# Kernel tuning notes

Hardware: AMD Instinct MI355X
Metric: run time of the kernel (lower is better)

## Reference

```python
import jax, jax.numpy as jnp
import numpy as np

KNN = 16
EPS = 1e-5

def _bn(x, g, b):
    # BatchNorm2d over channel-last axis, training-mode batch stats (axes B,N,K)
    m = jnp.mean(x, axis=(0, 1, 2), keepdims=True)
    v = jnp.var(x, axis=(0, 1, 2), keepdims=True)
    return (x - m) * jax.lax.rsqrt(v + EPS) * g + b

def _gather(x, idx):
    # x [B,N,C], idx [B,...] -> [B,...,C]
    return jax.vmap(lambda xi, ii: xi[ii])(x, idx)

def _fps(pc, m):
    # deterministic farthest point sampling starting at index 0 -> [B,m] int32
    B, N, _ = pc.shape
    first = jnp.zeros((B,), jnp.int32)
    def body(carry, _):
        mind, last = carry
        lp = jnp.take_along_axis(pc, last[:, None, None], axis=1)  # [B,1,3]
        mind = jnp.minimum(mind, jnp.sum((pc - lp) ** 2, axis=-1))  # [B,N]
        nxt = jnp.argmax(mind, axis=-1).astype(jnp.int32)
        return (mind, nxt), nxt
    _, rest = jax.lax.scan(body, (jnp.full((B, N), 1e10, pc.dtype), first), None, length=m - 1)
    return jnp.concatenate([first[None], rest], axis=0).T  # [B,m]

def _knn(pc1, pc2, k):
    # squared-distance matrix + k smallest (sorted ascending) -> indices [B,N1,k]
    d = (jnp.sum(pc1 ** 2, -1)[:, :, None] + jnp.sum(pc2 ** 2, -1)[:, None, :]
         - 2.0 * jnp.einsum('bnc,bmc->bnm', pc1, pc2))
    return jax.lax.top_k(-d, k)[1]

def reference(dec_x, dec_pc, enc_x, enc_pc,
              W_pre1, b_pre1, W_pre2, b_pre2,
              Wq, bq, Wk, bk, Wv, bv,
              Wp1, bp1, gp, betap, Wp2, bp2,
              Wa1, ba1, ga, betaa, Wa2, ba2,
              W_post1, b_post1, W_post2, b_post2):
    residue = dec_x
    dx = dec_x @ W_pre1 + b_pre1
    ex = enc_x @ W_pre2 + b_pre2
    pc = jnp.concatenate([dec_pc, enc_pc], axis=1)
    xx = jnp.concatenate([dx, ex], axis=1)
    fidx = _fps(pc, dec_pc.shape[1])
    pc = _gather(pc, fidx)
    xx = _gather(xx, fidx)
    q = dx @ Wq + bq
    k = xx @ Wk + bk
    v = xx @ Wv + bv
    nidx = _knn(dec_pc, pc, KNN)                          # [B,N1,K]
    pos_in = _gather(pc, nidx) - dec_pc[:, :, None, :]    # [B,N1,K,3] relative pos
    k = _gather(k, nidx)                                  # [B,N1,K,D]
    v = _gather(v, nidx)
    pos = jax.nn.relu(_bn(pos_in @ Wp1 + bp1, gp, betap)) @ Wp2 + bp2
    attn = k - q[:, :, None, :] + pos
    attn = jax.nn.relu(_bn(attn @ Wa1 + ba1, ga, betaa)) @ Wa2 + ba2
    attn = jax.nn.softmax(attn, axis=-2)                  # softmax over K neighbors
    x = jnp.sum((v + pos) * attn, axis=2)                 # [B,N1,D]
    return (x @ W_post1 + b_post1 + residue, dec_pc, x @ W_post2 + b_post2, enc_pc)

def setup_inputs():
    B, N1, N2 = 4, 2048, 2048
    D, I1, I2, HP, HA = 256, 256, 256, 64, 64
    ks = jax.random.split(jax.random.key(0), 24)
    rn = lambda i, shp, s: jax.random.normal(ks[i], shp, jnp.float32) * s
    z = lambda n: jnp.zeros((n,), jnp.float32)
    o = lambda n: jnp.ones((n,), jnp.float32)
    return {
        'dec_x': rn(0, (B, N1, I1), 1.0),
        'dec_pc': jax.random.uniform(ks[1], (B, N1, 3), jnp.float32),
        'enc_x': rn(2, (B, N2, I2), 1.0),
        'enc_pc': jax.random.uniform(ks[3], (B, N2, 3), jnp.float32),
        'W_pre1': rn(4, (I1, D), 0.02), 'b_pre1': z(D),
        'W_pre2': rn(5, (I2, D), 0.02), 'b_pre2': z(D),
        'Wq': rn(6, (D, D), 0.02), 'bq': z(D),
        'Wk': rn(7, (D, D), 0.02), 'bk': z(D),
        'Wv': rn(8, (D, D), 0.02), 'bv': z(D),
        'Wp1': rn(9, (3, HP), 0.1), 'bp1': z(HP), 'gp': o(HP), 'betap': z(HP),
        'Wp2': rn(10, (HP, D), 0.02), 'bp2': z(D),
        'Wa1': rn(11, (D, HA), 0.02), 'ba1': z(HA), 'ga': o(HA), 'betaa': z(HA),
        'Wa2': rn(12, (HA, D), 0.02), 'ba2': z(D),
        'W_post1': rn(13, (D, I1), 0.02), 'b_post1': z(I1),
        'W_post2': rn(14, (D, I2), 0.02), 'b_post2': z(I2),
    }
```

## Files before the change

### kernel.cpp

```cpp
#include <hip/hip_runtime.h>
#include <hip/hip_bf16.h>


typedef __hip_bfloat16 bf16;

__device__ __forceinline__ float b2f(bf16 x){ return __bfloat162float(x); }
__device__ __forceinline__ bf16  f2b(float x){ return __float2bfloat16(x); }

#define NQ    8192
#define NSAMP 131072

__global__ void detect_dtype(const unsigned int* __restrict__ words,
                             int* __restrict__ flag)
{
  int i = blockIdx.x*256 + threadIdx.x;
  unsigned int w = words[i];
  float v = __uint_as_float((w & 0xffffu) << 16);
  if (!(fabsf(v) <= 1e3f)) atomicOr(flag, 1);
}

struct ConvArgs {
  const void* src[30];
  float*      dst[30];
  int         n[30];
};
__global__ void convert_inputs(ConvArgs a, const int* __restrict__ flag)
{
  int t = blockIdx.y;
  int n = a.n[t];
  int isf32 = *flag;
  const void* s = a.src[t];
  float* d = a.dst[t];
  for (int i = blockIdx.x*256 + threadIdx.x; i < n; i += gridDim.x*256) {
    d[i] = isf32 ? ((const float*)s)[i] : b2f(((const bf16*)s)[i]);
  }
}

struct SGemm { float As[16][68]; float Bs[16][68]; };
struct SFps  { float sx[4096]; float sy[4096]; float sz[4096]; float2 slot[2][4]; };
union  SMega { SGemm g; SFps f; };

__device__ __forceinline__ void gemm_body(
    SGemm& sm, const float* __restrict__ A, const float* __restrict__ W,
    const float* __restrict__ bias, const float* __restrict__ resid,
    float* __restrict__ C, int N, int bm, int bn)
{
  int tid = threadIdx.x;
  int tr = tid >> 4, tc = tid & 15;
  float acc[4][4] = {};
  for (int k0 = 0; k0 < 256; k0 += 16) {
#pragma unroll
    for (int i = 0; i < 4; ++i) {
      int idx = tid + i*256;
      int m = idx >> 4, k = idx & 15;
      sm.As[k][m] = A[(size_t)(bm+m)*256 + k0 + k];
    }
#pragma unroll
    for (int i = 0; i < 4; ++i) {
      int idx = tid + i*256;
      int k = idx >> 6, n = idx & 63;
      sm.Bs[k][n] = W[(size_t)(k0+k)*N + bn + n];
    }
    __syncthreads();
#pragma unroll
    for (int k = 0; k < 16; ++k) {
      float4 a4 = *(const float4*)&sm.As[k][tr*4];
      float4 b4 = *(const float4*)&sm.Bs[k][tc*4];
      float a[4] = {a4.x, a4.y, a4.z, a4.w};
      float b[4] = {b4.x, b4.y, b4.z, b4.w};
#pragma unroll
      for (int i = 0; i < 4; ++i)
#pragma unroll
        for (int j = 0; j < 4; ++j) acc[i][j] += a[i]*b[j];
    }
    __syncthreads();
  }
#pragma unroll
  for (int i = 0; i < 4; ++i) {
    int m = bm + tr*4 + i;
#pragma unroll
    for (int j = 0; j < 4; ++j) {
      int n = bn + tc*4 + j;
      float v = acc[i][j];
      if (bias)  v += bias[n];
      if (resid) v += resid[(size_t)m*N + n];
      C[(size_t)m*N + n] = v;
    }
  }
}

template<int CTRL>
__device__ __forceinline__ void dpp_step(float& d, int& i) {
  int sd = __builtin_amdgcn_update_dpp(__float_as_int(d), __float_as_int(d),
                                       CTRL, 0xf, 0xf, false);
  int si = __builtin_amdgcn_update_dpp(i, i, CTRL, 0xf, 0xf, false);
  float fd = __int_as_float(sd);
  bool take = (fd > d) || (fd == d && si < i);
  d = take ? fd : d;
  i = take ? si : i;
}

__device__ void fps_body(SFps& sm, int b,
                         const float* __restrict__ dec_pc,
                         const float* __restrict__ enc_pc,
                         int* __restrict__ fidx)
{
  int tid = threadIdx.x;
  float px[16], py[16], pz[16], mind[16];
#pragma unroll
  for (int i = 0; i < 16; ++i) {
    int p = tid*16 + i;
    const float* s = (p < 2048) ? dec_pc + ((size_t)b*2048 + p)*3
                                : enc_pc + ((size_t)b*2048 + (p-2048))*3;
    px[i] = s[0]; py[i] = s[1]; pz[i] = s[2];
    sm.sx[p] = px[i]; sm.sy[p] = py[i]; sm.sz[p] = pz[i];
    mind[i] = 1e10f;
  }
  if (tid == 0) fidx[(size_t)b*2048] = 0;
  __syncthreads();

  int last = 0;
  int wv = tid >> 6;
  for (int t = 1; t < 2048; ++t) {
    float lx = sm.sx[last], ly = sm.sy[last], lz = sm.sz[last];
#pragma unroll
    for (int i = 0; i < 16; ++i) {
      float ddx = px[i]-lx, ddy = py[i]-ly, ddz = pz[i]-lz;
      float d = __fadd_rn(__fadd_rn(__fmul_rn(ddx,ddx), __fmul_rn(ddy,ddy)),
                          __fmul_rn(ddz,ddz));
      mind[i] = fminf(mind[i], d);
    }
    float vd[8]; int vi[8];
#pragma unroll
    for (int j = 0; j < 8; ++j) {
      bool tk = mind[j+8] > mind[j];
      vd[j] = tk ? mind[j+8] : mind[j];
      vi[j] = tk ? (j+8) : j;
    }
#pragma unroll
    for (int j = 0; j < 4; ++j) {
      bool tk = vd[j+4] > vd[j];
      vd[j] = tk ? vd[j+4] : vd[j];
      vi[j] = tk ? vi[j+4] : vi[j];
    }
#pragma unroll
    for (int j = 0; j < 2; ++j) {
      bool tk = vd[j+2] > vd[j];
      vd[j] = tk ? vd[j+2] : vd[j];
      vi[j] = tk ? vi[j+2] : vi[j];
    }
    bool tk0 = vd[1] > vd[0];
    float bv = tk0 ? vd[1] : vd[0];
    int   bi = tid*16 + (tk0 ? vi[1] : vi[0]);
    dpp_step<0x111>(bv, bi);
    dpp_step<0x112>(bv, bi);
    dpp_step<0x114>(bv, bi);
    dpp_step<0x118>(bv, bi);
    dpp_step<0x142>(bv, bi);
    dpp_step<0x143>(bv, bi);
    int par = t & 1;
    if ((tid & 63) == 63) sm.slot[par][wv] = make_float2(bv, __int_as_float(bi));
    __syncthreads();
    float4 s01 = *(const float4*)&sm.slot[par][0];
    float4 s23 = *(const float4*)&sm.slot[par][2];
    float d0 = s01.x; int i0 = __float_as_int(s01.y);
    float d1 = s01.z; int i1 = __float_as_int(s01.w);
    float d2 = s23.x; int i2 = __float_as_int(s23.y);
    float d3 = s23.z; int i3 = __float_as_int(s23.w);
    if (d1 > d0) { d0 = d1; i0 = i1; }
    if (d3 > d2) { d2 = d3; i2 = i3; }
    if (d2 > d0) { d0 = d2; i0 = i2; }
    last = i0;
    if (tid == 0) fidx[(size_t)b*2048 + t] = i0;
  }
}

struct Mega1Args {
  const float *dec_pc, *enc_pc, *dec_x, *enc_x;
  const float *WfV1, *WfV2, *WfQ, *WfK1, *WfK2;
  const float *bfV1, *bfV2, *bfQ, *bfK1, *bfK2;
  float *vdec, *venc, *qab, *kdec, *kenc;
  float *out1, *out3;
  int *fidx;
};
__global__ __launch_bounds__(256) void mega1(Mega1Args a)
{
  __shared__ SMega sm;
  int id = blockIdx.x;
  if (id < 4) {
    fps_body(sm.f, id, a.dec_pc, a.enc_pc, a.fidx);
  } else if (id < 516) {
    int l = id - 4;
    gemm_body(sm.g, a.dec_x, a.WfV1, a.bfV1, nullptr, a.vdec, 256,
              (l & 127) << 6, (l >> 7) << 6);
  } else if (id < 1028) {
    int l = id - 516;
    gemm_body(sm.g, a.enc_x, a.WfV2, a.bfV2, nullptr, a.venc, 256,
              (l & 127) << 6, (l >> 7) << 6);
  } else if (id < 1156) {
    int l = id - 1028;
    gemm_body(sm.g, a.dec_x, a.WfQ, a.bfQ, nullptr, a.qab, 64, l << 6, 0);
  } else if (id < 1284) {
    int l = id - 1156;
    gemm_body(sm.g, a.dec_x, a.WfK1, a.bfK1, nullptr, a.kdec, 64, l << 6, 0);
  } else if (id < 1412) {
    int l = id - 1284;
    gemm_body(sm.g, a.enc_x, a.WfK2, a.bfK2, nullptr, a.kenc, 64, l << 6, 0);
  } else if (id < 1508) {
    int i = (id - 1412)*256 + threadIdx.x;
    a.out1[i] = a.dec_pc[i];
  } else {
    int i = (id - 1508)*256 + threadIdx.x;
    a.out3[i] = a.enc_pc[i];
  }
}

__global__ __launch_bounds__(64) void foldA(
    const float* __restrict__ Wq, const float* __restrict__ bq,
    const float* __restrict__ Wk, const float* __restrict__ bk,
    const float* __restrict__ Wa1,
    const float* __restrict__ Wp2, const float* __restrict__ bp2,
    const float* __restrict__ ba1,
    float* __restrict__ Wqa, float* __restrict__ Wka,
    float* __restrict__ bqa, float* __restrict__ bka,
    float* __restrict__ Wpr, float* __restrict__ c1)
{
  int c = threadIdx.x;
  int r = blockIdx.x;
  if (r < 257) {
    float aq = 0.f, ak = 0.f;
    if (r < 256) {
      for (int j = 0; j < 256; ++j) {
        float w = Wa1[j*64+c];
        aq += Wq[r*256+j]*w; ak += Wk[r*256+j]*w;
      }
      Wqa[r*64+c] = aq; Wka[r*64+c] = ak;
    } else {
      for (int j = 0; j < 256; ++j) {
        float w = Wa1[j*64+c];
        aq += bq[j]*w; ak += bk[j]*w;
      }
      bqa[c] = aq; bka[c] = ak;
    }
  } else {
    int rr = r - 257;
    if (rr < 64) {
      float acc = 0.f;
      for (int e = 0; e < 256; ++e) acc += Wp2[rr*256+e] * Wa1[e*64+c];
      Wpr[rr*64+c] = acc;
    } else {
      float acc = ba1[c];
      for (int e = 0; e < 256; ++e) acc += bp2[e] * Wa1[e*64+c];
      c1[c] = acc;
    }
  }
}

struct FoldBArgs {
  const float *W_pre1, *W_pre2, *Wv, *Wqa, *Wka;
  const float *b_pre1, *b_pre2, *bv, *bqa, *bka;
  float *WfV1, *WfV2, *WfQ, *WfK1, *WfK2;
  float *bfV1, *bfV2, *bfQ, *bfK1, *bfK2;
};
__global__ __launch_bounds__(256) void foldB(FoldBArgs a)
{
  __shared__ SGemm sm;
  int id = blockIdx.x;
  if (id < 16) {
    gemm_body(sm, a.W_pre1, a.Wv, nullptr, nullptr, a.WfV1, 256,
              (id & 3) << 6, (id >> 2) << 6);
  } else if (id < 32) {
    int l = id - 16;
    gemm_body(sm, a.W_pre2, a.Wv, nullptr, nullptr, a.WfV2, 256,
              (l & 3) << 6, (l >> 2) << 6);
  } else if (id < 36) {
    gemm_body(sm, a.W_pre1, a.Wqa, nullptr, nullptr, a.WfQ, 64, (id-32) << 6, 0);
  } else if (id < 40) {
    gemm_body(sm, a.W_pre1, a.Wka, nullptr, nullptr, a.WfK1, 64, (id-36) << 6, 0);
  } else if (id < 44) {
    gemm_body(sm, a.W_pre2, a.Wka, nullptr, nullptr, a.WfK2, 64, (id-40) << 6, 0);
  } else {
    int t = threadIdx.x;
    float s1 = 0.f, s2 = 0.f;
    for (int k = 0; k < 256; ++k) {
      float w = a.Wv[k*256+t];
      s1 += a.b_pre1[k]*w; s2 += a.b_pre2[k]*w;
    }
    a.bfV1[t] = s1 + a.bv[t];
    a.bfV2[t] = s2 + a.bv[t];
    if (t < 64) {
      float q = 0.f, k1 = 0.f, k2 = 0.f;
      for (int k = 0; k < 256; ++k) {
        float wq = a.Wqa[k*64+t], wk = a.Wka[k*64+t];
        q  += a.b_pre1[k]*wq;
        k1 += a.b_pre1[k]*wk;
        k2 += a.b_pre2[k]*wk;
      }
      a.bfQ[t]  = q  + a.bqa[t];
      a.bfK1[t] = k1 + a.bka[t];
      a.bfK2[t] = k2 + a.bka[t];
    }
  }
}

__global__ __launch_bounds__(64) void gfetch(
    const float* __restrict__ vdec, const float* __restrict__ venc,
    const float* __restrict__ kdec, const float* __restrict__ kenc,
    const float* __restrict__ dec_pc, const float* __restrict__ enc_pc,
    const int* __restrict__ fidx,
    float* __restrict__ vsb, float* __restrict__ kab, float* __restrict__ pcs)
{
  int id = blockIdx.x;
  if (id < 8192) {
    int r = id;
    int b = r >> 11;
    int g = fidx[r];
    const float* vsrc = (g < 2048) ? vdec + ((size_t)(b*2048 + g))*256
                                   : venc + ((size_t)(b*2048 + g - 2048))*256;
    ((float4*)(vsb + (size_t)r*256))[threadIdx.x] = ((const float4*)vsrc)[threadIdx.x];
    const float* ksrc = (g < 2048) ? kdec + (size_t)(b*2048 + g)*64
                                   : kenc + (size_t)(b*2048 + g - 2048)*64;
    kab[(size_t)r*64 + threadIdx.x] = ksrc[threadIdx.x];
  } else {
    int i = (id - 8192)*64 + threadIdx.x;
    int b = i >> 11;
    int g = fidx[i];
    const float* s = (g < 2048) ? dec_pc + ((size_t)b*2048 + g)*3
                                : enc_pc + ((size_t)b*2048 + (g-2048))*3;
    float X = s[0], Y = s[1], Z = s[2];
    float s2 = __fadd_rn(__fadd_rn(__fmul_rn(X,X), __fmul_rn(Y,Y)), __fmul_rn(Z,Z));
    ((float4*)pcs)[i] = make_float4(X, Y, Z, s2);
  }
}

__global__ __launch_bounds__(64) void knn_kernel(
    const float* __restrict__ dec_pc, const float* __restrict__ pcs,
    int* __restrict__ nidx)
{
  int gq = blockIdx.x*64 + threadIdx.x;
  if (gq >= NQ) return;
  int b = gq >> 11;
  float qx = dec_pc[(size_t)gq*3+0];
  float qy = dec_pc[(size_t)gq*3+1];
  float qz = dec_pc[(size_t)gq*3+2];
  float s1 = __fadd_rn(__fadd_rn(__fmul_rn(qx,qx), __fmul_rn(qy,qy)), __fmul_rn(qz,qz));
  float bd[16]; int bi[16];
#pragma unroll
  for (int i = 0; i < 16; ++i) { bd[i] = 3.4e38f; bi[i] = 0; }
  const float4* P = (const float4*)(pcs) + (size_t)b*2048;
  for (int j = 0; j < 2048; ++j) {
    float4 p = P[j];
    float inner = __fadd_rn(__fadd_rn(__fmul_rn(qx,p.x), __fmul_rn(qy,p.y)),
                            __fmul_rn(qz,p.z));
    float d = __fsub_rn(__fadd_rn(s1, p.w), __fmul_rn(2.f, inner));
    if (d < bd[15]) {
      bd[15] = d; bi[15] = j;
#pragma unroll
      for (int k = 15; k >= 1; --k) {
        if (bd[k] < bd[k-1]) {
          float td = bd[k]; bd[k] = bd[k-1]; bd[k-1] = td;
          int   ti = bi[k]; bi[k] = bi[k-1]; bi[k-1] = ti;
        }
      }
    }
  }
  int* o = nidx + (size_t)gq*16;
#pragma unroll
  for (int i = 0; i < 16; ++i) o[i] = bi[i];
}

__global__ __launch_bounds__(256) void bn1_stats(
    const float* __restrict__ dec_pc, const float* __restrict__ pcs,
    const int* __restrict__ nidx, const float* __restrict__ Wp1,
    const float* __restrict__ bp1, double* __restrict__ sums)
{
  __shared__ float pin[256][3];
  __shared__ float red[8][64];
  int tid = threadIdx.x;
  int s0 = blockIdx.x * 256;
  {
    int s = s0 + tid;
    int qrow = s >> 4;
    int b = s >> 15;
    int g = nidx[s];
    float4 p = ((const float4*)pcs)[(size_t)b*2048 + g];
    pin[tid][0] = p.x - dec_pc[(size_t)qrow*3+0];
    pin[tid][1] = p.y - dec_pc[(size_t)qrow*3+1];
    pin[tid][2] = p.z - dec_pc[(size_t)qrow*3+2];
  }
  __syncthreads();
  int c = tid & 63, grp = tid >> 6;
  float w0 = Wp1[c], w1 = Wp1[64+c], w2 = Wp1[128+c], bb = bp1[c];
  float sm = 0.f, sq = 0.f;
  for (int i = 0; i < 64; ++i) {
    int r = grp*64 + i;
    float h = pin[r][0]*w0 + pin[r][1]*w1 + pin[r][2]*w2 + bb;
    sm += h; sq += h*h;
  }
  red[grp][c] = sm; red[4+grp][c] = sq;
  __syncthreads();
  if (tid < 64) {
    atomicAdd(&sums[tid], (double)(red[0][tid]+red[1][tid]+red[2][tid]+red[3][tid]));
  } else if (tid < 128) {
    int c2 = tid - 64;
    atomicAdd(&sums[64+c2], (double)(red[4][c2]+red[5][c2]+red[6][c2]+red[7][c2]));
  }
}

__global__ void bn_fin(const double* __restrict__ sums,
                       const float* __restrict__ gamma, const float* __restrict__ beta,
                       float* __restrict__ ab)
{
  int c = threadIdx.x;
  double mean = sums[c]    * (1.0/131072.0);
  double var  = sums[64+c] * (1.0/131072.0) - mean*mean;
  double inv  = 1.0 / sqrt(var + 1e-5);
  float a  = (float)(gamma[c] * inv);
  float bb = (float)(beta[c] - mean * (double)a);
  ab[c] = a; ab[64+c] = bb;
}

__global__ __launch_bounds__(256) void ph_kernel(
    const float* __restrict__ dec_pc, const float* __restrict__ pcs,
    const int* __restrict__ nidx, const float* __restrict__ Wp1,
    const float* __restrict__ bp1, const float* __restrict__ ab,
    bf16* __restrict__ PH)
{
  __shared__ float pin[256][3];
  int tid = threadIdx.x;
  int s0 = blockIdx.x * 256;
  {
    int s = s0 + tid;
    int qrow = s >> 4;
    int b = s >> 15;
    int g = nidx[s];
    float4 p = ((const float4*)pcs)[(size_t)b*2048 + g];
    pin[tid][0] = p.x - dec_pc[(size_t)qrow*3+0];
    pin[tid][1] = p.y - dec_pc[(size_t)qrow*3+1];
    pin[tid][2] = p.z - dec_pc[(size_t)qrow*3+2];
  }
  __syncthreads();
  int c = tid & 63, grp = tid >> 6;
  float w0 = Wp1[c], w1 = Wp1[64+c], w2 = Wp1[128+c], bb = bp1[c];
  float a = ab[c], sh = ab[64+c];
  for (int i = 0; i < 64; ++i) {
    int r = grp*64 + i;
    int s = s0 + r;
    float h = pin[r][0]*w0 + pin[r][1]*w1 + pin[r][2]*w2 + bb;
    PH[(size_t)s*64 + c] = f2b(fmaxf(h*a + sh, 0.f));
  }
}

__global__ __launch_bounds__(256) void bn2_stats(
    const bf16* __restrict__ PH, const float* __restrict__ Wpr,
    const float* __restrict__ ka, const float* __restrict__ qa,
    const float* __restrict__ c1v, const int* __restrict__ nidx,
    bf16* __restrict__ attnpre, double* __restrict__ sums)
{
  __shared__ float phT[64][68];
  __shared__ float wp[64][68];
  __shared__ float red[16][64];
  __shared__ float red2[16][64];
  int tid = threadIdx.x;
  int s0 = blockIdx.x * 64;
#pragma unroll
  for (int i = 0; i < 16; ++i) {
    int idx = tid + i*256;
    wp[idx>>6][idx&63] = Wpr[idx];
    int r = idx >> 6, d = idx & 63;
    phT[d][r] = b2f(PH[(size_t)(s0+r)*64 + d]);
  }
  __syncthreads();
  int tr = tid >> 4, tc = tid & 15;
  float acc[4][4] = {};
#pragma unroll 8
  for (int d = 0; d < 64; ++d) {
    float4 a4 = *(const float4*)&phT[d][tr*4];
    float4 b4 = *(const float4*)&wp[d][tc*4];
    float a[4] = {a4.x, a4.y, a4.z, a4.w};
    float b[4] = {b4.x, b4.y, b4.z, b4.w};
#pragma unroll
    for (int i = 0; i < 4; ++i)
#pragma unroll
      for (int j = 0; j < 4; ++j) acc[i][j] += a[i]*b[j];
  }
  float psum[4] = {0,0,0,0}, psq[4] = {0,0,0,0};
#pragma unroll
  for (int i = 0; i < 4; ++i) {
    int r = tr*4 + i;
    int s = s0 + r;
    int qrow = s >> 4;
    const float* karow = ka + (size_t)s*64;
    const float* qarow = qa + (size_t)qrow*64;
    (void)karow;
#pragma unroll
    for (int j = 0; j < 4; ++j) {
      int c = tc*4 + j;
      int b = s >> 15;
      int g = nidx[s];
      float v = acc[i][j] + ka[((size_t)(b*2048 + g))*64 + c] - qarow[c] + c1v[c];
      attnpre[(size_t)s*64 + c] = f2b(v);
      psum[j] += v; psq[j] += v*v;
    }
  }
#pragma unroll
  for (int j = 0; j < 4; ++j) { red[tr][tc*4+j] = psum[j]; red2[tr][tc*4+j] = psq[j]; }
  __syncthreads();
  if (tid < 64) {
    float t = 0.f, t2 = 0.f;
#pragma unroll
    for (int i = 0; i < 16; ++i) { t += red[i][tid]; t2 += red2[i][tid]; }
    atomicAdd(&sums[tid], (double)t);
    atomicAdd(&sums[64+tid], (double)t2);
  }
}

__global__ __launch_bounds__(256) void final_attn(
    const bf16* __restrict__ attnpre, const bf16* __restrict__ PH,
    const float* __restrict__ ab2,
    const float* __restrict__ Wa2, const float* __restrict__ ba2,
    const float* __restrict__ Wp2, const float* __restrict__ bp2,
    const float* __restrict__ vsb, const int* __restrict__ nidx,
    float* __restrict__ xout)
{
  int tid = threadIdx.x;
  float wa[64], wpc[64];
#pragma unroll
  for (int d = 0; d < 64; ++d) {
    wa[d]  = Wa2[d*256 + tid];
    wpc[d] = Wp2[d*256 + tid];
  }
  float cba2 = ba2[tid];
  float cbp2 = bp2[tid];
  __shared__ float th[16][64];
  __shared__ float ph[16][64];
  __shared__ int   sn[16];
  for (int qi = 0; qi < 16; ++qi) {
    int q = blockIdx.x*16 + qi;
#pragma unroll
    for (int i = 0; i < 4; ++i) {
      int idx = tid + i*256;
      int k = idx >> 6, d = idx & 63;
      size_t gi = (size_t)q*1024 + idx;
      th[k][d] = fmaxf(b2f(attnpre[gi])*ab2[d] + ab2[64+d], 0.f);
      ph[k][d] = b2f(PH[gi]);
    }
    if (tid < 16) sn[tid] = nidx[(size_t)q*16 + tid];
    __syncthreads();
    float av[16], pv[16];
#pragma unroll
    for (int k = 0; k < 16; ++k) {
      float sa = cba2, sp = cbp2;
#pragma unroll
      for (int d = 0; d < 64; d += 4) {
        float4 t4 = *(const float4*)&th[k][d];
        float4 p4 = *(const float4*)&ph[k][d];
        sa += t4.x*wa[d] + t4.y*wa[d+1] + t4.z*wa[d+2] + t4.w*wa[d+3];
        sp += p4.x*wpc[d] + p4.y*wpc[d+1] + p4.z*wpc[d+2] + p4.w*wpc[d+3];
      }
      av[k] = sa; pv[k] = sp;
    }
    float m = av[0];
#pragma unroll
    for (int k = 1; k < 16; ++k) m = fmaxf(m, av[k]);
    float den = 0.f, num = 0.f;
    int b = q >> 11;
#pragma unroll
    for (int k = 0; k < 16; ++k) {
      float e = __expf(av[k] - m);
      den += e;
      float vk = vsb[((size_t)(b*2048 + sn[k]))*256 + tid];
      num += (vk + pv[k]) * e;
    }
    xout[(size_t)q*256 + tid] = num / den;
    __syncthreads();
  }
}

struct PostArgs {
  const float *xb, *Wp1_, *bp1_, *Wp2_, *bp2_, *resid;
  float *o1, *o2;
};
__global__ __launch_bounds__(256) void mega_post(PostArgs a)
{
  __shared__ SGemm sm;
  int id = blockIdx.x;
  if (id < 512) {
    gemm_body(sm, a.xb, a.Wp1_, a.bp1_, a.resid, a.o1, 256,
              (id & 127) << 6, (id >> 7) << 6);
  } else {
    int l = id - 512;
    gemm_body(sm, a.xb, a.Wp2_, a.bp2_, nullptr, a.o2, 256,
              (l & 127) << 6, (l >> 7) << 6);
  }
}

extern "C" void kernel_launch(void* const* d_in, const int* in_sizes, int n_in,
                              void* d_out, int out_size, void* d_ws, size_t ws_size,
                              hipStream_t stream) {
  (void)in_sizes; (void)n_in; (void)out_size; (void)ws_size;
  char* ws = (char*)d_ws;

  float* vdec    = (float*)(ws + 0);
  float* venc    = (float*)(ws + 8388608);
  float* vsb     = (float*)(ws + 16777216);
  float* xb      = (float*)(ws + 25165824);
  float* dec_xF  = (float*)(ws + 33554432);
  float* enc_xF  = (float*)(ws + 41943040);
  bf16*  PHb     = (bf16*)(ws + 50331648);
  bf16*  apre    = (bf16*)(ws + 67108864);
  float* qab     = (float*)(ws + 83886080);
  float* kab     = (float*)(ws + 85983232);
  float* kdec    = (float*)(ws + 88080384);
  float* kenc    = (float*)(ws + 90177536);
  float* dec_pcF = (float*)(ws + 92274688);
  float* enc_pcF = (float*)(ws + 92372992);
  float* W_pre1F = (float*)(ws + 92471296);
  float* W_pre2F = (float*)(ws + 92733440);
  float* WqF     = (float*)(ws + 92995584);
  float* WkF     = (float*)(ws + 93257728);
  float* WvF     = (float*)(ws + 93519872);
  float* W_post1F= (float*)(ws + 93782016);
  float* W_post2F= (float*)(ws + 94044160);
  float* Wp2F    = (float*)(ws + 94306304);
  float* Wa1F    = (float*)(ws + 94371840);
  float* Wa2F    = (float*)(ws + 94437376);
  float* Wp1F    = (float*)(ws + 94502912);
  float* vecs    = (float*)(ws + 94503680);
  float* b_pre1F = vecs + 0*256;
  float* b_pre2F = vecs + 1*256;
  float* bqF     = vecs + 2*256;
  float* bkF     = vecs + 3*256;
  float* bvF     = vecs + 4*256;
  float* bp1F    = vecs + 5*256;
  float* gpF     = vecs + 6*256;
  float* betapF  = vecs + 7*256;
  float* bp2F    = vecs + 8*256;
  float* ba1F    = vecs + 9*256;
  float* gaF     = vecs + 10*256;
  float* betaaF  = vecs + 11*256;
  float* ba2F    = vecs + 12*256;
  float* b_post1F= vecs + 13*256;
  float* b_post2F= vecs + 14*256;
  float* WfV1    = (float*)(ws + 94519040);
  float* WfV2    = (float*)(ws + 94781184);
  float* WfQ     = (float*)(ws + 95043328);
  float* WfK1    = (float*)(ws + 95108864);
  float* WfK2    = (float*)(ws + 95174400);
  float* Wqa     = (float*)(ws + 95239936);
  float* Wka     = (float*)(ws + 95305472);
  float* bfV1    = (float*)(ws + 95371008);
  float* bfV2    = (float*)(ws + 95372032);
  float* bfQ     = (float*)(ws + 95373056);
  float* bfK1    = (float*)(ws + 95373312);
  float* bfK2    = (float*)(ws + 95373568);
  float* bqa     = (float*)(ws + 95373824);
  float* bka     = (float*)(ws + 95374080);
  float* pcs     = (float*)(ws + 95374336);
  int*   fidx    = (int*)(ws + 95505408);
  int*   nidx    = (int*)(ws + 95538176);
  double* sums   = (double*)(ws + 96062464);
  float* Wpr     = (float*)(ws + 96064512);
  float* c1v     = (float*)(ws + 96080896);
  float* a1b1    = (float*)(ws + 96081152);
  float* a2b2    = (float*)(ws + 96081664);
  int*   flag    = (int*)(ws + 96082176);

  float* out  = (float*)d_out;
  float* out1 = out + 2097152;
  float* out2 = out + 2121728;
  float* out3 = out + 4218880;

  hipMemsetAsync(sums, 0, 256*sizeof(double), stream);
  hipMemsetAsync(flag, 0, sizeof(int), stream);

  detect_dtype<<<64, 256, 0, stream>>>((const unsigned int*)d_in[2], flag);

  ConvArgs ca;
  const int ns[30] = {2097152,24576,2097152,24576, 65536,256,65536,256,
                      65536,256,65536,256,65536,256, 192,64,64,64,
                      16384,256,16384,64,64,64,16384,256,
                      65536,256,65536,256};
  float* dsts[30] = {dec_xF,dec_pcF,enc_xF,enc_pcF, W_pre1F,b_pre1F,W_pre2F,b_pre2F,
                     WqF,bqF,WkF,bkF,WvF,bvF, Wp1F,bp1F,gpF,betapF,
                     Wp2F,bp2F,Wa1F,ba1F,gaF,betaaF,Wa2F,ba2F,
                     W_post1F,b_post1F,W_post2F,b_post2F};
  for (int i = 0; i < 30; ++i) { ca.src[i] = d_in[i]; ca.dst[i] = dsts[i]; ca.n[i] = ns[i]; }
  convert_inputs<<<dim3(512, 30), 256, 0, stream>>>(ca, flag);

  foldA<<<322, 64, 0, stream>>>(WqF, bqF, WkF, bkF, Wa1F, Wp2F, bp2F, ba1F,
                                Wqa, Wka, bqa, bka, Wpr, c1v);

  FoldBArgs fb;
  fb.W_pre1 = W_pre1F; fb.W_pre2 = W_pre2F; fb.Wv = WvF; fb.Wqa = Wqa; fb.Wka = Wka;
  fb.b_pre1 = b_pre1F; fb.b_pre2 = b_pre2F; fb.bv = bvF; fb.bqa = bqa; fb.bka = bka;
  fb.WfV1 = WfV1; fb.WfV2 = WfV2; fb.WfQ = WfQ; fb.WfK1 = WfK1; fb.WfK2 = WfK2;
  fb.bfV1 = bfV1; fb.bfV2 = bfV2; fb.bfQ = bfQ; fb.bfK1 = bfK1; fb.bfK2 = bfK2;
  foldB<<<45, 256, 0, stream>>>(fb);

  Mega1Args m1;
  m1.dec_pc = dec_pcF; m1.enc_pc = enc_pcF; m1.dec_x = dec_xF; m1.enc_x = enc_xF;
  m1.WfV1 = WfV1; m1.WfV2 = WfV2; m1.WfQ = WfQ; m1.WfK1 = WfK1; m1.WfK2 = WfK2;
  m1.bfV1 = bfV1; m1.bfV2 = bfV2; m1.bfQ = bfQ; m1.bfK1 = bfK1; m1.bfK2 = bfK2;
  m1.vdec = vdec; m1.venc = venc; m1.qab = qab; m1.kdec = kdec; m1.kenc = kenc;
  m1.out1 = out1; m1.out3 = out3; m1.fidx = fidx;
  mega1<<<1604, 256, 0, stream>>>(m1);

  gfetch<<<8320, 64, 0, stream>>>(vdec, venc, kdec, kenc, dec_pcF, enc_pcF,
                                  fidx, vsb, kab, pcs);
  knn_kernel<<<128, 64, 0, stream>>>(dec_pcF, pcs, nidx);

  bn1_stats<<<512, 256, 0, stream>>>(dec_pcF, pcs, nidx, Wp1F, bp1F, sums);
  bn_fin<<<1, 64, 0, stream>>>(sums, gpF, betapF, a1b1);
  ph_kernel<<<512, 256, 0, stream>>>(dec_pcF, pcs, nidx, Wp1F, bp1F, a1b1, PHb);

  bn2_stats<<<2048, 256, 0, stream>>>(PHb, Wpr, kab, qab, c1v, nidx, apre, sums + 128);
  bn_fin<<<1, 64, 0, stream>>>(sums + 128, gaF, betaaF, a2b2);

  final_attn<<<512, 256, 0, stream>>>(apre, PHb, a2b2, Wa2F, ba2F, Wp2F, bp2F,
                                      vsb, nidx, xb);

  PostArgs pa;
  pa.xb = xb; pa.Wp1_ = W_post1F; pa.bp1_ = b_post1F;
  pa.Wp2_ = W_post2F; pa.bp2_ = b_post2F; pa.resid = dec_xF;
  pa.o1 = out; pa.o2 = out2;
  mega_post<<<1024, 256, 0, stream>>>(pa);
}
```

Baseline: 2.765 ms.

## Use 512-thread blocks for FPS and GEMMs and fold BN finalization into consumers

Farthest point sampling now runs with 512 threads, each owning 8 points instead of 16, so each serial iteration has shorter per-thread min and argmax chains. Point coordinates are packed as float4 in shared memory and the next point is fetched right after the cross-wave reduction. FPS also raises its wave priority with s_setprio. The shared GEMM body is remapped to 512 threads computing 2x4 outputs each, so the mega1, foldB and mega_post launches change to 512 threads. The two tiny bn_fin kernels are removed and their mean/variance finalization is recomputed inside ph_kernel and final_attn, saving two launches. The cost is a wider block barrier across 8 waves per FPS step and duplicated per-thread double-precision finalization.

```diff
diff --git a/kernel.cpp b/kernel.cpp
--- a/kernel.cpp
+++ b/kernel.cpp
@@ -37,7 +37,10 @@
 }
 
 struct SGemm { float As[16][68]; float Bs[16][68]; };
-struct SFps  { float sx[4096]; float sy[4096]; float sz[4096]; float2 slot[2][4]; };
+struct SFps  {
+  float4 spc[4096];
+  __align__(16) float2 slot[2][8];
+};
 union  SMega { SGemm g; SFps f; };
 
 __device__ __forceinline__ void gemm_body(
@@ -47,37 +50,33 @@
 {
   int tid = threadIdx.x;
   int tr = tid >> 4, tc = tid & 15;
-  float acc[4][4] = {};
+  float acc[2][4] = {};
   for (int k0 = 0; k0 < 256; k0 += 16) {
 #pragma unroll
-    for (int i = 0; i < 4; ++i) {
-      int idx = tid + i*256;
+    for (int i = 0; i < 2; ++i) {
+      int idx = tid + i*512;
       int m = idx >> 4, k = idx & 15;
       sm.As[k][m] = A[(size_t)(bm+m)*256 + k0 + k];
-    }
-#pragma unroll
-    for (int i = 0; i < 4; ++i) {
-      int idx = tid + i*256;
-      int k = idx >> 6, n = idx & 63;
-      sm.Bs[k][n] = W[(size_t)(k0+k)*N + bn + n];
+      int kb = idx >> 6, n = idx & 63;
+      sm.Bs[kb][n] = W[(size_t)(k0+kb)*N + bn + n];
     }
     __syncthreads();
 #pragma unroll
     for (int k = 0; k < 16; ++k) {
-      float4 a4 = *(const float4*)&sm.As[k][tr*4];
+      float2 a2 = *(const float2*)&sm.As[k][tr*2];
       float4 b4 = *(const float4*)&sm.Bs[k][tc*4];
-      float a[4] = {a4.x, a4.y, a4.z, a4.w};
+      float a[2] = {a2.x, a2.y};
       float b[4] = {b4.x, b4.y, b4.z, b4.w};
 #pragma unroll
-      for (int i = 0; i < 4; ++i)
+      for (int i = 0; i < 2; ++i)
 #pragma unroll
         for (int j = 0; j < 4; ++j) acc[i][j] += a[i]*b[j];
     }
     __syncthreads();
   }
 #pragma unroll
-  for (int i = 0; i < 4; ++i) {
-    int m = bm + tr*4 + i;
+  for (int i = 0; i < 2; ++i) {
+    int m = bm + tr*2 + i;
 #pragma unroll
     for (int j = 0; j < 4; ++j) {
       int n = bn + tc*4 + j;
@@ -105,53 +104,51 @@
                          const float* __restrict__ enc_pc,
                          int* __restrict__ fidx)
 {
+#if defined(__has_builtin)
+#if __has_builtin(__builtin_amdgcn_s_setprio)
+  __builtin_amdgcn_s_setprio(3);
+#endif
+#endif
   int tid = threadIdx.x;
-  float px[16], py[16], pz[16], mind[16];
-#pragma unroll
-  for (int i = 0; i < 16; ++i) {
-    int p = tid*16 + i;
+  float px[8], py[8], pz[8], mind[8];
+#pragma unroll
+  for (int i = 0; i < 8; ++i) {
+    int p = tid*8 + i;
     const float* s = (p < 2048) ? dec_pc + ((size_t)b*2048 + p)*3
                                 : enc_pc + ((size_t)b*2048 + (p-2048))*3;
     px[i] = s[0]; py[i] = s[1]; pz[i] = s[2];
-    sm.sx[p] = px[i]; sm.sy[p] = py[i]; sm.sz[p] = pz[i];
+    sm.spc[p] = make_float4(px[i], py[i], pz[i], 0.f);
     mind[i] = 1e10f;
   }
   if (tid == 0) fidx[(size_t)b*2048] = 0;
   __syncthreads();
-
-  int last = 0;
+  float4 w = sm.spc[0];
   int wv = tid >> 6;
   for (int t = 1; t < 2048; ++t) {
-    float lx = sm.sx[last], ly = sm.sy[last], lz = sm.sz[last];
-#pragma unroll
-    for (int i = 0; i < 16; ++i) {
-      float ddx = px[i]-lx, ddy = py[i]-ly, ddz = pz[i]-lz;
+#pragma unroll
+    for (int i = 0; i < 8; ++i) {
+      float ddx = px[i]-w.x, ddy = py[i]-w.y, ddz = pz[i]-w.z;
       float d = __fadd_rn(__fadd_rn(__fmul_rn(ddx,ddx), __fmul_rn(ddy,ddy)),
                           __fmul_rn(ddz,ddz));
       mind[i] = fminf(mind[i], d);
     }
-    float vd[8]; int vi[8];
-#pragma unroll
-    for (int j = 0; j < 8; ++j) {
-      bool tk = mind[j+8] > mind[j];
-      vd[j] = tk ? mind[j+8] : mind[j];
-      vi[j] = tk ? (j+8) : j;
-    }
+    float vd[4]; int vi[4];
 #pragma unroll
     for (int j = 0; j < 4; ++j) {
-      bool tk = vd[j+4] > vd[j];
-      vd[j] = tk ? vd[j+4] : vd[j];
-      vi[j] = tk ? vi[j+4] : vi[j];
-    }
+      bool tk = mind[2*j+1] > mind[2*j];
+      vd[j] = tk ? mind[2*j+1] : mind[2*j];
+      vi[j] = tk ? 2*j+1 : 2*j;
+    }
+    float ud[2]; int ui[2];
 #pragma unroll
     for (int j = 0; j < 2; ++j) {
-      bool tk = vd[j+2] > vd[j];
-      vd[j] = tk ? vd[j+2] : vd[j];
-      vi[j] = tk ? vi[j+2] : vi[j];
-    }
-    bool tk0 = vd[1] > vd[0];
-    float bv = tk0 ? vd[1] : vd[0];
-    int   bi = tid*16 + (tk0 ? vi[1] : vi[0]);
+      bool tk = vd[2*j+1] > vd[2*j];
+      ud[j] = tk ? vd[2*j+1] : vd[2*j];
+      ui[j] = tk ? vi[2*j+1] : vi[2*j];
+    }
+    bool tk0 = ud[1] > ud[0];
+    float bv = tk0 ? ud[1] : ud[0];
+    int   bi = tid*8 + (tk0 ? ui[1] : ui[0]);
     dpp_step<0x111>(bv, bi);
     dpp_step<0x112>(bv, bi);
     dpp_step<0x114>(bv, bi);
@@ -161,18 +158,31 @@
     int par = t & 1;
     if ((tid & 63) == 63) sm.slot[par][wv] = make_float2(bv, __int_as_float(bi));
     __syncthreads();
-    float4 s01 = *(const float4*)&sm.slot[par][0];
-    float4 s23 = *(const float4*)&sm.slot[par][2];
+    const float4* sp = (const float4*)&sm.slot[par][0];
+    float4 s01 = sp[0], s23 = sp[1], s45 = sp[2], s67 = sp[3];
     float d0 = s01.x; int i0 = __float_as_int(s01.y);
     float d1 = s01.z; int i1 = __float_as_int(s01.w);
     float d2 = s23.x; int i2 = __float_as_int(s23.y);
     float d3 = s23.z; int i3 = __float_as_int(s23.w);
+    float d4 = s45.x; int i4 = __float_as_int(s45.y);
+    float d5 = s45.z; int i5 = __float_as_int(s45.w);
+    float d6 = s67.x; int i6 = __float_as_int(s67.y);
+    float d7 = s67.z; int i7 = __float_as_int(s67.w);
     if (d1 > d0) { d0 = d1; i0 = i1; }
     if (d3 > d2) { d2 = d3; i2 = i3; }
+    if (d5 > d4) { d4 = d5; i4 = i5; }
+    if (d7 > d6) { d6 = d7; i6 = i7; }
     if (d2 > d0) { d0 = d2; i0 = i2; }
-    last = i0;
+    if (d6 > d4) { d4 = d6; i4 = i6; }
+    if (d4 > d0) { d0 = d4; i0 = i4; }
     if (tid == 0) fidx[(size_t)b*2048 + t] = i0;
-  }
+    w = sm.spc[i0];
+  }
+#if defined(__has_builtin)
+#if __has_builtin(__builtin_amdgcn_s_setprio)
+  __builtin_amdgcn_s_setprio(0);
+#endif
+#endif
 }
 
 struct Mega1Args {
@@ -183,7 +193,7 @@
   float *out1, *out3;
   int *fidx;
 };
-__global__ __launch_bounds__(256) void mega1(Mega1Args a)
+__global__ __launch_bounds__(512) void mega1(Mega1Args a)
 {
   __shared__ SMega sm;
   int id = blockIdx.x;
@@ -206,11 +216,11 @@
   } else if (id < 1412) {
     int l = id - 1284;
     gemm_body(sm.g, a.enc_x, a.WfK2, a.bfK2, nullptr, a.kenc, 64, l << 6, 0);
-  } else if (id < 1508) {
-    int i = (id - 1412)*256 + threadIdx.x;
+  } else if (id < 1460) {
+    int i = (id - 1412)*512 + threadIdx.x;
     a.out1[i] = a.dec_pc[i];
   } else {
-    int i = (id - 1508)*256 + threadIdx.x;
+    int i = (id - 1460)*512 + threadIdx.x;
     a.out3[i] = a.enc_pc[i];
   }
 }
@@ -262,7 +272,7 @@
   float *WfV1, *WfV2, *WfQ, *WfK1, *WfK2;
   float *bfV1, *bfV2, *bfQ, *bfK1, *bfK2;
 };
-__global__ __launch_bounds__(256) void foldB(FoldBArgs a)
+__global__ __launch_bounds__(512) void foldB(FoldBArgs a)
 {
   __shared__ SGemm sm;
   int id = blockIdx.x;
@@ -281,24 +291,26 @@
     gemm_body(sm, a.W_pre2, a.Wka, nullptr, nullptr, a.WfK2, 64, (id-40) << 6, 0);
   } else {
     int t = threadIdx.x;
-    float s1 = 0.f, s2 = 0.f;
-    for (int k = 0; k < 256; ++k) {
-      float w = a.Wv[k*256+t];
-      s1 += a.b_pre1[k]*w; s2 += a.b_pre2[k]*w;
-    }
-    a.bfV1[t] = s1 + a.bv[t];
-    a.bfV2[t] = s2 + a.bv[t];
-    if (t < 64) {
-      float q = 0.f, k1 = 0.f, k2 = 0.f;
+    if (t < 256) {
+      float s1 = 0.f, s2 = 0.f;
       for (int k = 0; k < 256; ++k) {
-        float wq = a.Wqa[k*64+t], wk = a.Wka[k*64+t];
-        q  += a.b_pre1[k]*wq;
-        k1 += a.b_pre1[k]*wk;
-        k2 += a.b_pre2[k]*wk;
+        float w = a.Wv[k*256+t];
+        s1 += a.b_pre1[k]*w; s2 += a.b_pre2[k]*w;
       }
-      a.bfQ[t]  = q  + a.bqa[t];
-      a.bfK1[t] = k1 + a.bka[t];
-      a.bfK2[t] = k2 + a.bka[t];
+      a.bfV1[t] = s1 + a.bv[t];
+      a.bfV2[t] = s2 + a.bv[t];
+      if (t < 64) {
+        float q = 0.f, k1 = 0.f, k2 = 0.f;
+        for (int k = 0; k < 256; ++k) {
+          float wq = a.Wqa[k*64+t], wk = a.Wka[k*64+t];
+          q  += a.b_pre1[k]*wq;
+          k1 += a.b_pre1[k]*wk;
+          k2 += a.b_pre2[k]*wk;
+        }
+        a.bfQ[t]  = q  + a.bqa[t];
+        a.bfK1[t] = k1 + a.bka[t];
+        a.bfK2[t] = k2 + a.bka[t];
+      }
     }
   }
 }
@@ -407,23 +419,11 @@
   }
 }
 
-__global__ void bn_fin(const double* __restrict__ sums,
-                       const float* __restrict__ gamma, const float* __restrict__ beta,
-                       float* __restrict__ ab)
-{
-  int c = threadIdx.x;
-  double mean = sums[c]    * (1.0/131072.0);
-  double var  = sums[64+c] * (1.0/131072.0) - mean*mean;
-  double inv  = 1.0 / sqrt(var + 1e-5);
-  float a  = (float)(gamma[c] * inv);
-  float bb = (float)(beta[c] - mean * (double)a);
-  ab[c] = a; ab[64+c] = bb;
-}
-
 __global__ __launch_bounds__(256) void ph_kernel(
     const float* __restrict__ dec_pc, const float* __restrict__ pcs,
     const int* __restrict__ nidx, const float* __restrict__ Wp1,
-    const float* __restrict__ bp1, const float* __restrict__ ab,
+    const float* __restrict__ bp1, const double* __restrict__ sums,
+    const float* __restrict__ gamma, const float* __restrict__ beta,
     bf16* __restrict__ PH)
 {
   __shared__ float pin[256][3];
@@ -442,7 +442,11 @@
   __syncthreads();
   int c = tid & 63, grp = tid >> 6;
   float w0 = Wp1[c], w1 = Wp1[64+c], w2 = Wp1[128+c], bb = bp1[c];
-  float a = ab[c], sh = ab[64+c];
+  double mean = sums[c]    * (1.0/131072.0);
+  double var  = sums[64+c] * (1.0/131072.0) - mean*mean;
+  double inv  = 1.0 / sqrt(var + 1e-5);
+  float a  = (float)(gamma[c] * inv);
+  float sh = (float)(beta[c] - mean * (double)a);
   for (int i = 0; i < 64; ++i) {
     int r = grp*64 + i;
     int s = s0 + r;
@@ -490,9 +494,7 @@
     int r = tr*4 + i;
     int s = s0 + r;
     int qrow = s >> 4;
-    const float* karow = ka + (size_t)s*64;
     const float* qarow = qa + (size_t)qrow*64;
-    (void)karow;
 #pragma unroll
     for (int j = 0; j < 4; ++j) {
       int c = tc*4 + j;
@@ -517,13 +519,21 @@
 
 __global__ __launch_bounds__(256) void final_attn(
     const bf16* __restrict__ attnpre, const bf16* __restrict__ PH,
-    const float* __restrict__ ab2,
+    const double* __restrict__ sums2,
+    const float* __restrict__ ga, const float* __restrict__ betaa,
     const float* __restrict__ Wa2, const float* __restrict__ ba2,
     const float* __restrict__ Wp2, const float* __restrict__ bp2,
     const float* __restrict__ vsb, const int* __restrict__ nidx,
     float* __restrict__ xout)
 {
   int tid = threadIdx.x;
+  int c = tid & 63;
+  double mean = sums2[c]    * (1.0/131072.0);
+  double var  = sums2[64+c] * (1.0/131072.0) - mean*mean;
+  double inv  = 1.0 / sqrt(var + 1e-5);
+  float a2 = (float)(ga[c] * inv);
+  float s2 = (float)(betaa[c] - mean * (double)a2);
+
   float wa[64], wpc[64];
 #pragma unroll
   for (int d = 0; d < 64; ++d) {
@@ -542,7 +552,7 @@
       int idx = tid + i*256;
       int k = idx >> 6, d = idx & 63;
       size_t gi = (size_t)q*1024 + idx;
-      th[k][d] = fmaxf(b2f(attnpre[gi])*ab2[d] + ab2[64+d], 0.f);
+      th[k][d] = fmaxf(b2f(attnpre[gi])*a2 + s2, 0.f);
       ph[k][d] = b2f(PH[gi]);
     }
     if (tid < 16) sn[tid] = nidx[(size_t)q*16 + tid];
@@ -581,7 +591,7 @@
   const float *xb, *Wp1_, *bp1_, *Wp2_, *bp2_, *resid;
   float *o1, *o2;
 };
-__global__ __launch_bounds__(256) void mega_post(PostArgs a)
+__global__ __launch_bounds__(512) void mega_post(PostArgs a)
 {
   __shared__ SGemm sm;
   int id = blockIdx.x;
@@ -662,8 +672,6 @@
   double* sums   = (double*)(ws + 96062464);
   float* Wpr     = (float*)(ws + 96064512);
   float* c1v     = (float*)(ws + 96080896);
-  float* a1b1    = (float*)(ws + 96081152);
-  float* a2b2    = (float*)(ws + 96081664);
   int*   flag    = (int*)(ws + 96082176);
 
   float* out  = (float*)d_out;
@@ -696,7 +704,7 @@
   fb.b_pre1 = b_pre1F; fb.b_pre2 = b_pre2F; fb.bv = bvF; fb.bqa = bqa; fb.bka = bka;
   fb.WfV1 = WfV1; fb.WfV2 = WfV2; fb.WfQ = WfQ; fb.WfK1 = WfK1; fb.WfK2 = WfK2;
   fb.bfV1 = bfV1; fb.bfV2 = bfV2; fb.bfQ = bfQ; fb.bfK1 = bfK1; fb.bfK2 = bfK2;
-  foldB<<<45, 256, 0, stream>>>(fb);
+  foldB<<<45, 512, 0, stream>>>(fb);
 
   Mega1Args m1;
   m1.dec_pc = dec_pcF; m1.enc_pc = enc_pcF; m1.dec_x = dec_xF; m1.enc_x = enc_xF;
@@ -704,25 +712,24 @@
   m1.bfV1 = bfV1; m1.bfV2 = bfV2; m1.bfQ = bfQ; m1.bfK1 = bfK1; m1.bfK2 = bfK2;
   m1.vdec = vdec; m1.venc = venc; m1.qab = qab; m1.kdec = kdec; m1.kenc = kenc;
   m1.out1 = out1; m1.out3 = out3; m1.fidx = fidx;
-  mega1<<<1604, 256, 0, stream>>>(m1);
+  mega1<<<1508, 512, 0, stream>>>(m1);
 
   gfetch<<<8320, 64, 0, stream>>>(vdec, venc, kdec, kenc, dec_pcF, enc_pcF,
                                   fidx, vsb, kab, pcs);
   knn_kernel<<<128, 64, 0, stream>>>(dec_pcF, pcs, nidx);
 
   bn1_stats<<<512, 256, 0, stream>>>(dec_pcF, pcs, nidx, Wp1F, bp1F, sums);
-  bn_fin<<<1, 64, 0, stream>>>(sums, gpF, betapF, a1b1);
-  ph_kernel<<<512, 256, 0, stream>>>(dec_pcF, pcs, nidx, Wp1F, bp1F, a1b1, PHb);
+  ph_kernel<<<512, 256, 0, stream>>>(dec_pcF, pcs, nidx, Wp1F, bp1F,
+                                     sums, gpF, betapF, PHb);
 
   bn2_stats<<<2048, 256, 0, stream>>>(PHb, Wpr, kab, qab, c1v, nidx, apre, sums + 128);
-  bn_fin<<<1, 64, 0, stream>>>(sums + 128, gaF, betaaF, a2b2);
-
-  final_attn<<<512, 256, 0, stream>>>(apre, PHb, a2b2, Wa2F, ba2F, Wp2F, bp2F,
-                                      vsb, nidx, xb);
+
+  final_attn<<<512, 256, 0, stream>>>(apre, PHb, sums + 128, gaF, betaaF,
+                                      Wa2F, ba2F, Wp2F, bp2F, vsb, nidx, xb);
 
   PostArgs pa;
   pa.xb = xb; pa.Wp1_ = W_post1F; pa.bp1_ = b_post1F;
   pa.Wp2_ = W_post2F; pa.bp2_ = b_post2F; pa.resid = dec_xF;
   pa.o1 = out; pa.o2 = out2;
-  mega_post<<<1024, 256, 0, stream>>>(pa);
-}
+  mega_post<<<1024, 512, 0, stream>>>(pa);
+}
```

Result: slower. 2.851 ms (+3.1%).

## Carry FPS winner coordinates through argmax reduction and fold BN finalize into consumers

Applied to the files above, without the earlier changes.

The farthest-point-sampling argmax reduction now carries the winning point's xyz coordinates alongside its distance and index, through the in-thread tree, the DPP steps and the cross-wave LDS slots. This removes the dependent shared-memory lookup of the selected point at the start of each of the 2047 serial iterations. The cost is extra register moves and three more DPP shuffles per step. The FPS block also raises its wave priority with s_setprio. Separately, the two single-block bn_fin launches are removed and the mean/variance finalization is recomputed inside ph_kernel and final_attn, saving two kernel launches at the price of redundant per-thread double-precision math.

```diff
diff --git a/kernel.cpp b/kernel.cpp
--- a/kernel.cpp
+++ b/kernel.cpp
@@ -37,7 +37,11 @@
 }
 
 struct SGemm { float As[16][68]; float Bs[16][68]; };
-struct SFps  { float sx[4096]; float sy[4096]; float sz[4096]; float2 slot[2][4]; };
+struct SFps  {
+  float4 spc[4096];
+  __align__(16) float4 slotC[2][4];
+  __align__(16) int    slotI[2][4];
+};
 union  SMega { SGemm g; SFps f; };
 
 __device__ __forceinline__ void gemm_body(
@@ -90,14 +94,24 @@
 }
 
 template<int CTRL>
-__device__ __forceinline__ void dpp_step(float& d, int& i) {
+__device__ __forceinline__ void dpp_step5(float& d, int& i,
+                                          float& x, float& y, float& z) {
   int sd = __builtin_amdgcn_update_dpp(__float_as_int(d), __float_as_int(d),
                                        CTRL, 0xf, 0xf, false);
   int si = __builtin_amdgcn_update_dpp(i, i, CTRL, 0xf, 0xf, false);
+  int sx = __builtin_amdgcn_update_dpp(__float_as_int(x), __float_as_int(x),
+                                       CTRL, 0xf, 0xf, false);
+  int sy = __builtin_amdgcn_update_dpp(__float_as_int(y), __float_as_int(y),
+                                       CTRL, 0xf, 0xf, false);
+  int sz = __builtin_amdgcn_update_dpp(__float_as_int(z), __float_as_int(z),
+                                       CTRL, 0xf, 0xf, false);
   float fd = __int_as_float(sd);
   bool take = (fd > d) || (fd == d && si < i);
   d = take ? fd : d;
   i = take ? si : i;
+  x = take ? __int_as_float(sx) : x;
+  y = take ? __int_as_float(sy) : y;
+  z = take ? __int_as_float(sz) : z;
 }
 
 __device__ void fps_body(SFps& sm, int b,
@@ -105,6 +119,11 @@
                          const float* __restrict__ enc_pc,
                          int* __restrict__ fidx)
 {
+#if defined(__has_builtin)
+#if __has_builtin(__builtin_amdgcn_s_setprio)
+  __builtin_amdgcn_s_setprio(3);
+#endif
+#endif
   int tid = threadIdx.x;
   float px[16], py[16], pz[16], mind[16];
 #pragma unroll
@@ -113,66 +132,87 @@
     const float* s = (p < 2048) ? dec_pc + ((size_t)b*2048 + p)*3
                                 : enc_pc + ((size_t)b*2048 + (p-2048))*3;
     px[i] = s[0]; py[i] = s[1]; pz[i] = s[2];
-    sm.sx[p] = px[i]; sm.sy[p] = py[i]; sm.sz[p] = pz[i];
+    sm.spc[p] = make_float4(px[i], py[i], pz[i], 0.f);
     mind[i] = 1e10f;
   }
   if (tid == 0) fidx[(size_t)b*2048] = 0;
   __syncthreads();
-
-  int last = 0;
+  float4 w0 = sm.spc[0];
+  float wx = w0.x, wy = w0.y, wz = w0.z;
   int wv = tid >> 6;
   for (int t = 1; t < 2048; ++t) {
-    float lx = sm.sx[last], ly = sm.sy[last], lz = sm.sz[last];
 #pragma unroll
     for (int i = 0; i < 16; ++i) {
-      float ddx = px[i]-lx, ddy = py[i]-ly, ddz = pz[i]-lz;
+      float ddx = px[i]-wx, ddy = py[i]-wy, ddz = pz[i]-wz;
       float d = __fadd_rn(__fadd_rn(__fmul_rn(ddx,ddx), __fmul_rn(ddy,ddy)),
                           __fmul_rn(ddz,ddz));
       mind[i] = fminf(mind[i], d);
     }
-    float vd[8]; int vi[8];
+    float d8[8], x8[8], y8[8], z8[8]; int i8[8];
 #pragma unroll
     for (int j = 0; j < 8; ++j) {
-      bool tk = mind[j+8] > mind[j];
-      vd[j] = tk ? mind[j+8] : mind[j];
-      vi[j] = tk ? (j+8) : j;
-    }
+      bool tk = mind[2*j+1] > mind[2*j];
+      d8[j] = tk ? mind[2*j+1] : mind[2*j];
+      i8[j] = tk ? 2*j+1 : 2*j;
+      x8[j] = tk ? px[2*j+1] : px[2*j];
+      y8[j] = tk ? py[2*j+1] : py[2*j];
+      z8[j] = tk ? pz[2*j+1] : pz[2*j];
+    }
+    float d4[4], x4[4], y4[4], z4[4]; int i4[4];
 #pragma unroll
     for (int j = 0; j < 4; ++j) {
-      bool tk = vd[j+4] > vd[j];
-      vd[j] = tk ? vd[j+4] : vd[j];
-      vi[j] = tk ? vi[j+4] : vi[j];
-    }
+      bool tk = d8[2*j+1] > d8[2*j];
+      d4[j] = tk ? d8[2*j+1] : d8[2*j];
+      i4[j] = tk ? i8[2*j+1] : i8[2*j];
+      x4[j] = tk ? x8[2*j+1] : x8[2*j];
+      y4[j] = tk ? y8[2*j+1] : y8[2*j];
+      z4[j] = tk ? z8[2*j+1] : z8[2*j];
+    }
+    float d2[2], x2[2], y2[2], z2[2]; int i2[2];
 #pragma unroll
     for (int j = 0; j < 2; ++j) {
-      bool tk = vd[j+2] > vd[j];
-      vd[j] = tk ? vd[j+2] : vd[j];
-      vi[j] = tk ? vi[j+2] : vi[j];
-    }
-    bool tk0 = vd[1] > vd[0];
-    float bv = tk0 ? vd[1] : vd[0];
-    int   bi = tid*16 + (tk0 ? vi[1] : vi[0]);
-    dpp_step<0x111>(bv, bi);
-    dpp_step<0x112>(bv, bi);
-    dpp_step<0x114>(bv, bi);
-    dpp_step<0x118>(bv, bi);
-    dpp_step<0x142>(bv, bi);
-    dpp_step<0x143>(bv, bi);
+      bool tk = d4[2*j+1] > d4[2*j];
+      d2[j] = tk ? d4[2*j+1] : d4[2*j];
+      i2[j] = tk ? i4[2*j+1] : i4[2*j];
+      x2[j] = tk ? x4[2*j+1] : x4[2*j];
+      y2[j] = tk ? y4[2*j+1] : y4[2*j];
+      z2[j] = tk ? z4[2*j+1] : z4[2*j];
+    }
+    bool tk0 = d2[1] > d2[0];
+    float bv = tk0 ? d2[1] : d2[0];
+    int   bi = tid*16 + (tk0 ? i2[1] : i2[0]);
+    float bx = tk0 ? x2[1] : x2[0];
+    float by = tk0 ? y2[1] : y2[0];
+    float bz = tk0 ? z2[1] : z2[0];
+    dpp_step5<0x111>(bv, bi, bx, by, bz);
+    dpp_step5<0x112>(bv, bi, bx, by, bz);
+    dpp_step5<0x114>(bv, bi, bx, by, bz);
+    dpp_step5<0x118>(bv, bi, bx, by, bz);
+    dpp_step5<0x142>(bv, bi, bx, by, bz);
+    dpp_step5<0x143>(bv, bi, bx, by, bz);
     int par = t & 1;
-    if ((tid & 63) == 63) sm.slot[par][wv] = make_float2(bv, __int_as_float(bi));
+    if ((tid & 63) == 63) {
+      sm.slotC[par][wv] = make_float4(bx, by, bz, bv);
+      sm.slotI[par][wv] = bi;
+    }
     __syncthreads();
-    float4 s01 = *(const float4*)&sm.slot[par][0];
-    float4 s23 = *(const float4*)&sm.slot[par][2];
-    float d0 = s01.x; int i0 = __float_as_int(s01.y);
-    float d1 = s01.z; int i1 = __float_as_int(s01.w);
-    float d2 = s23.x; int i2 = __float_as_int(s23.y);
-    float d3 = s23.z; int i3 = __float_as_int(s23.w);
-    if (d1 > d0) { d0 = d1; i0 = i1; }
-    if (d3 > d2) { d2 = d3; i2 = i3; }
-    if (d2 > d0) { d0 = d2; i0 = i2; }
-    last = i0;
-    if (tid == 0) fidx[(size_t)b*2048 + t] = i0;
-  }
+    float4 c0 = sm.slotC[par][0];
+    float4 c1 = sm.slotC[par][1];
+    float4 c2 = sm.slotC[par][2];
+    float4 c3 = sm.slotC[par][3];
+    int4   ii = *(const int4*)&sm.slotI[par][0];
+    int j0 = ii.x, j1 = ii.y, j2 = ii.z, j3 = ii.w;
+    if (c1.w > c0.w) { c0 = c1; j0 = j1; }
+    if (c3.w > c2.w) { c2 = c3; j2 = j3; }
+    if (c2.w > c0.w) { c0 = c2; j0 = j2; }
+    wx = c0.x; wy = c0.y; wz = c0.z;
+    if (tid == 0) fidx[(size_t)b*2048 + t] = j0;
+  }
+#if defined(__has_builtin)
+#if __has_builtin(__builtin_amdgcn_s_setprio)
+  __builtin_amdgcn_s_setprio(0);
+#endif
+#endif
 }
 
 struct Mega1Args {
@@ -407,23 +447,11 @@
   }
 }
 
-__global__ void bn_fin(const double* __restrict__ sums,
-                       const float* __restrict__ gamma, const float* __restrict__ beta,
-                       float* __restrict__ ab)
-{
-  int c = threadIdx.x;
-  double mean = sums[c]    * (1.0/131072.0);
-  double var  = sums[64+c] * (1.0/131072.0) - mean*mean;
-  double inv  = 1.0 / sqrt(var + 1e-5);
-  float a  = (float)(gamma[c] * inv);
-  float bb = (float)(beta[c] - mean * (double)a);
-  ab[c] = a; ab[64+c] = bb;
-}
-
 __global__ __launch_bounds__(256) void ph_kernel(
     const float* __restrict__ dec_pc, const float* __restrict__ pcs,
     const int* __restrict__ nidx, const float* __restrict__ Wp1,
-    const float* __restrict__ bp1, const float* __restrict__ ab,
+    const float* __restrict__ bp1, const double* __restrict__ sums,
+    const float* __restrict__ gamma, const float* __restrict__ beta,
     bf16* __restrict__ PH)
 {
   __shared__ float pin[256][3];
@@ -442,7 +470,11 @@
   __syncthreads();
   int c = tid & 63, grp = tid >> 6;
   float w0 = Wp1[c], w1 = Wp1[64+c], w2 = Wp1[128+c], bb = bp1[c];
-  float a = ab[c], sh = ab[64+c];
+  double mean = sums[c]    * (1.0/131072.0);
+  double var  = sums[64+c] * (1.0/131072.0) - mean*mean;
+  double inv  = 1.0 / sqrt(var + 1e-5);
+  float a  = (float)(gamma[c] * inv);
+  float sh = (float)(beta[c] - mean * (double)a);
   for (int i = 0; i < 64; ++i) {
     int r = grp*64 + i;
     int s = s0 + r;
@@ -490,9 +522,7 @@
     int r = tr*4 + i;
     int s = s0 + r;
     int qrow = s >> 4;
-    const float* karow = ka + (size_t)s*64;
     const float* qarow = qa + (size_t)qrow*64;
-    (void)karow;
 #pragma unroll
     for (int j = 0; j < 4; ++j) {
       int c = tc*4 + j;
@@ -517,13 +547,21 @@
 
 __global__ __launch_bounds__(256) void final_attn(
     const bf16* __restrict__ attnpre, const bf16* __restrict__ PH,
-    const float* __restrict__ ab2,
+    const double* __restrict__ sums2,
+    const float* __restrict__ ga, const float* __restrict__ betaa,
     const float* __restrict__ Wa2, const float* __restrict__ ba2,
     const float* __restrict__ Wp2, const float* __restrict__ bp2,
     const float* __restrict__ vsb, const int* __restrict__ nidx,
     float* __restrict__ xout)
 {
   int tid = threadIdx.x;
+  int c = tid & 63;
+  double mean = sums2[c]    * (1.0/131072.0);
+  double var  = sums2[64+c] * (1.0/131072.0) - mean*mean;
+  double inv  = 1.0 / sqrt(var + 1e-5);
+  float a2 = (float)(ga[c] * inv);
+  float s2 = (float)(betaa[c] - mean * (double)a2);
+
   float wa[64], wpc[64];
 #pragma unroll
   for (int d = 0; d < 64; ++d) {
@@ -542,7 +580,7 @@
       int idx = tid + i*256;
       int k = idx >> 6, d = idx & 63;
       size_t gi = (size_t)q*1024 + idx;
-      th[k][d] = fmaxf(b2f(attnpre[gi])*ab2[d] + ab2[64+d], 0.f);
+      th[k][d] = fmaxf(b2f(attnpre[gi])*a2 + s2, 0.f);
       ph[k][d] = b2f(PH[gi]);
     }
     if (tid < 16) sn[tid] = nidx[(size_t)q*16 + tid];
@@ -662,8 +700,6 @@
   double* sums   = (double*)(ws + 96062464);
   float* Wpr     = (float*)(ws + 96064512);
   float* c1v     = (float*)(ws + 96080896);
-  float* a1b1    = (float*)(ws + 96081152);
-  float* a2b2    = (float*)(ws + 96081664);
   int*   flag    = (int*)(ws + 96082176);
 
   float* out  = (float*)d_out;
@@ -711,14 +747,13 @@
   knn_kernel<<<128, 64, 0, stream>>>(dec_pcF, pcs, nidx);
 
   bn1_stats<<<512, 256, 0, stream>>>(dec_pcF, pcs, nidx, Wp1F, bp1F, sums);
-  bn_fin<<<1, 64, 0, stream>>>(sums, gpF, betapF, a1b1);
-  ph_kernel<<<512, 256, 0, stream>>>(dec_pcF, pcs, nidx, Wp1F, bp1F, a1b1, PHb);
+  ph_kernel<<<512, 256, 0, stream>>>(dec_pcF, pcs, nidx, Wp1F, bp1F,
+                                     sums, gpF, betapF, PHb);
 
   bn2_stats<<<2048, 256, 0, stream>>>(PHb, Wpr, kab, qab, c1v, nidx, apre, sums + 128);
-  bn_fin<<<1, 64, 0, stream>>>(sums + 128, gaF, betaaF, a2b2);
-
-  final_attn<<<512, 256, 0, stream>>>(apre, PHb, a2b2, Wa2F, ba2F, Wp2F, bp2F,
-                                      vsb, nidx, xb);
+
+  final_attn<<<512, 256, 0, stream>>>(apre, PHb, sums + 128, gaF, betaaF,
+                                      Wa2F, ba2F, Wp2F, bp2F, vsb, nidx, xb);
 
   PostArgs pa;
   pa.xb = xb; pa.Wp1_ = W_post1F; pa.bp1_ = b_post1F;
```

After: 3.463 ms. 1.25x slower.
